# Optimization experiments

Hardware: AMD Instinct MI355X
Metric: run time of the kernel (lower is better)

The kernel has to match this reference:

```python
import jax, jax.numpy as jnp
import numpy as np

NUM_LAYERS = 3
CH = 8            # dynamic head channels
CIN = 8           # mask-branch feature channels
MASK_OUT_STRIDE = 4
WEIGHT_NUMS = [(CIN + 2) * CH, CH * CH, CH * 1]
BIAS_NUMS = [CH, CH, 1]
NUM_GEN_PARAMS = sum(WEIGHT_NUMS) + sum(BIAS_NUMS)  # 169


def compute_locations(h, w, stride):
    # FCOS-style pixel center locations, x-coordinate first: (H*W, 2)
    sx = jnp.arange(w, dtype=jnp.float32) * stride + stride // 2
    sy = jnp.arange(h, dtype=jnp.float32) * stride + stride // 2
    yy, xx = jnp.meshgrid(sy, sx, indexing='ij')
    return jnp.stack([xx.reshape(-1), yy.reshape(-1)], axis=1)


def _resize_axis_align_corners(x, factor, axis):
    # Bilinear, align_corners=True, out_size = factor*(in_size-1)+1.
    # Source coords are exactly j/factor, so interpolation weights are static.
    s = x.shape[axis] - 1
    j = jnp.arange(factor * s + 1)
    i0 = j // factor
    i1 = jnp.minimum(i0 + 1, s)
    frac = (j % factor).astype(x.dtype) / factor
    shp = [1] * x.ndim
    shp[axis] = -1
    frac = frac.reshape(shp)
    return jnp.take(x, i0, axis=axis) * (1 - frac) + jnp.take(x, i1, axis=axis) * frac


def aligned_bilinear(t, factor):
    if factor == 1:
        return t
    h, w = t.shape[2], t.shape[3]
    t = jnp.pad(t, ((0, 0), (0, 0), (0, 1), (0, 1)), mode='edge')   # replicate pad bottom/right
    t = _resize_axis_align_corners(t, factor, 2)                     # -> factor*h + 1
    t = _resize_axis_align_corners(t, factor, 3)                     # -> factor*w + 1
    p = factor // 2
    t = jnp.pad(t, ((0, 0), (0, 0), (p, 0), (p, 0)), mode='edge')    # replicate pad top/left
    return t[:, :, :factor * h, :factor * w]


def parse_params(params):
    # params: (n_inst, 169) -> per-instance weights/biases of the 3 1x1 conv layers
    n = params.shape[0]
    idx = np.cumsum(WEIGHT_NUMS + BIAS_NUMS)[:-1]
    w0, w1, w2, b0, b1, b2 = jnp.split(params, idx, axis=1)
    w0 = w0.reshape(n, CH, CIN + 2)
    w1 = w1.reshape(n, CH, CH)
    w2 = w2.reshape(n, 1, CH)
    b2 = b2.reshape(n, 1)
    return (w0, w1, w2), (b0, b1, b2)


def dynamic_mask_head(mask_feats, mask_head_params, locations, im_inds, fpn_levels, sizes_of_interest, mask_feat_stride):
    N, C, H, W = mask_feats.shape
    n_inst = mask_head_params.shape[0]
    locs = compute_locations(H, W, mask_feat_stride)                 # (HW, 2)
    rel = locations[:, None, :] - locs[None, :, :]                   # (n, HW, 2)
    rel = jnp.transpose(rel, (0, 2, 1))                              # (n, 2, HW)
    soi = sizes_of_interest[fpn_levels]                              # (n,)
    rel = (rel / soi[:, None, None]).astype(mask_feats.dtype)
    feats = mask_feats[im_inds].reshape(n_inst, CIN, H * W)          # gather per-instance image feats
    x = jnp.concatenate([rel, feats], axis=1)                        # (n, CIN+2, HW)
    (w0, w1, w2), (b0, b1, b2) = parse_params(mask_head_params)
    # grouped 1x1 convs (groups = n_inst) == per-instance small matmuls
    x = jax.nn.relu(jnp.einsum('noi,nip->nop', w0, x) + b0[:, :, None])
    x = jax.nn.relu(jnp.einsum('noi,nip->nop', w1, x) + b1[:, :, None])
    x = jnp.einsum('noi,nip->nop', w2, x) + b2[:, :, None]           # (n, 1, HW)
    logits = x.reshape(n_inst, 1, H, W)
    logits = aligned_bilinear(logits, mask_feat_stride // MASK_OUT_STRIDE)
    return jax.nn.sigmoid(logits)


def setup_inputs() -> dict:
    key = jax.random.key(0)
    k1, k2, k3, k4, k5 = jax.random.split(key, 5)
    N, H, W, n_inst = 2, 136, 200, 128
    mask_feats = jax.random.normal(k1, (N, CIN, H, W), dtype=jnp.float32)
    mask_head_params = jax.random.normal(k2, (n_inst, NUM_GEN_PARAMS), dtype=jnp.float32) * 0.1
    locations = jax.random.uniform(k3, (n_inst, 2), dtype=jnp.float32) * 1600.0
    im_inds = jax.random.randint(k4, (n_inst,), 0, N)
    fpn_levels = jax.random.randint(k5, (n_inst,), 0, 5)
    sizes_of_interest = jnp.array([64.0, 128.0, 256.0, 512.0, 1024.0], dtype=jnp.float32)
    return {"mask_feats": mask_feats, "mask_head_params": mask_head_params, "locations": locations,
            "im_inds": im_inds, "fpn_levels": fpn_levels, "sizes_of_interest": sizes_of_interest,
            "mask_feat_stride": 8}


def reference(mask_feats, mask_head_params, locations, im_inds, fpn_levels, sizes_of_interest, mask_feat_stride):
    return dynamic_mask_head(mask_feats, mask_head_params, locations, im_inds, fpn_levels,
                             sizes_of_interest, mask_feat_stride)
```

## Files before the change

### kernel.cpp

```cpp
#include <hip/hip_runtime.h>
#include <math.h>

typedef __fp16 h2 __attribute__((ext_vector_type(2)));

#define H_IN   136
#define W_IN   200
#define HWP    (H_IN * W_IN)
#define OH     272
#define OW     400
#define RB     8
#define NSTRIP 17
#define LROWS  (RB + 1)
#define CH     8
#define CIN    8
#define NPARAM 169
#define NEG_LOG2E (-1.4426950408889634f)



__device__ __forceinline__ h2 pkrtz(float a, float b) {
    return __builtin_amdgcn_cvt_pkrtz(a, b);
}

__global__ __launch_bounds__(256, 3) void mask_head_fused(
    const float* __restrict__ mask_feats,
    const float* __restrict__ params,
    const float* __restrict__ locations,
    const int*   __restrict__ im_inds,
    const int*   __restrict__ fpn_levels,
    const float* __restrict__ soi_tab,
    float* __restrict__ out)
{
    __shared__ h2    sW[NPARAM];
    __shared__ float T[LROWS][W_IN];

    const int inst = blockIdx.y;
    const int r0   = blockIdx.x * RB;
    const int tid  = threadIdx.x;

    const float* P = params + inst * NPARAM;
    if (tid < NPARAM) {
        float w = P[tid];
        if ((tid >= 144 && tid < 152) || tid == 168) w *= NEG_LOG2E;
        const __fp16 hw = (__fp16)w;
        h2 v; v.x = hw; v.y = hw;
        sW[tid] = v;
    }

    const float loc_x   = locations[2 * inst];
    const float loc_y   = locations[2 * inst + 1];
    const float inv_soi = 1.0f / soi_tab[fpn_levels[inst]];
    const float* F = mask_feats + (size_t)im_inds[inst] * (CIN * HWP);
    float* O = out + (size_t)inst * (OH * OW);
    __syncthreads();

    if (tid < LROWS * (W_IN / 8)) {
        const int k = tid / 25;
        const int c = (tid - k * 25) * 8;
        const int r = min(max(r0 - 1 + k, 0), H_IN - 1);

        h2 f[CIN][4];
        #pragma unroll
        for (int ch = 0; ch < CIN; ++ch) {
            const float* q = F + ch * HWP + r * W_IN + c;
            const float4 A = *(const float4*)q;
            const float4 B = *(const float4*)(q + 4);
            f[ch][0] = pkrtz(A.x, A.y); f[ch][1] = pkrtz(A.z, A.w);
            f[ch][2] = pkrtz(B.x, B.y); f[ch][3] = pkrtz(B.z, B.w);
        }

        const float ry  = (loc_y - (float)(r * 8 + 4)) * inv_soi;
        const float dx  = -8.0f * inv_soi;
        const float rx0 = (loc_x - (float)(c * 8 + 4)) * inv_soi;
        h2 rxh[4];
        #pragma unroll
        for (int s = 0; s < 4; ++s)
            rxh[s] = pkrtz(rx0 + (float)(2 * s) * dx, rx0 + (float)(2 * s + 1) * dx);
        const h2 ryh = pkrtz(ry, ry);
        const h2 z2  = {(__fp16)0.0f, (__fp16)0.0f};

        h2 h0[CH][4];
        #pragma unroll
        for (int o = 0; o < CH; ++o) {
            const h2 base = __builtin_elementwise_fma(sW[o * 10 + 1], ryh, sW[152 + o]);
            const h2 wx = sW[o * 10];
            h2 a[4];
            #pragma unroll
            for (int s = 0; s < 4; ++s) a[s] = __builtin_elementwise_fma(wx, rxh[s], base);
            #pragma unroll
            for (int i = 0; i < CIN; ++i) {
                const h2 w = sW[o * 10 + 2 + i];
                #pragma unroll
                for (int s = 0; s < 4; ++s) a[s] = __builtin_elementwise_fma(w, f[i][s], a[s]);
            }
            #pragma unroll
            for (int s = 0; s < 4; ++s) h0[o][s] = __builtin_elementwise_max(a[s], z2);
        }

        h2 h1[CH][4];
        #pragma unroll
        for (int o = 0; o < CH; ++o) {
            const h2 b = sW[160 + o];
            h2 a[4] = {b, b, b, b};
            #pragma unroll
            for (int i = 0; i < CH; ++i) {
                const h2 w = sW[80 + o * CH + i];
                #pragma unroll
                for (int s = 0; s < 4; ++s) a[s] = __builtin_elementwise_fma(w, h0[i][s], a[s]);
            }
            #pragma unroll
            for (int s = 0; s < 4; ++s) h1[o][s] = __builtin_elementwise_max(a[s], z2);
        }

        const h2 b2 = sW[168];
        h2 t[4] = {b2, b2, b2, b2};
        #pragma unroll
        for (int i = 0; i < CH; ++i) {
            const h2 w = sW[144 + i];
            #pragma unroll
            for (int s = 0; s < 4; ++s) t[s] = __builtin_elementwise_fma(w, h1[i][s], t[s]);
        }

        *(float4*)&T[k][c] = make_float4((float)t[0].x, (float)t[0].y,
                                         (float)t[1].x, (float)t[1].y);
        *(float4*)&T[k][c + 4] = make_float4((float)t[2].x, (float)t[2].y,
                                             (float)t[3].x, (float)t[3].y);
    }
    __syncthreads();

    #pragma unroll
    for (int it = 0; it < 2; ++it) {
        const int s = tid + 256 * it;
        if (s < RB * (W_IN / 4)) {
            const int rpl = s / (W_IN / 4);
            const int t   = s - rpl * (W_IN / 4);
            const int cm  = 4 * t;
            const int cl  = max(cm - 1, 0);

            const float4 mR = *(const float4*)&T[rpl + 1][cm];
            const float4 mQ = *(const float4*)&T[rpl][cm];
            const float  AR = T[rpl + 1][cl];
            const float  AQ = T[rpl][cl];

            const float Aa = 0.5f * (AR + AQ);
            const float Ba = 0.5f * (mR.x + mQ.x);
            const float Ca = 0.5f * (mR.y + mQ.y);
            const float Da = 0.5f * (mR.z + mQ.z);
            const float Ea = 0.5f * (mR.w + mQ.w);

            float4 s0, s1, s2, s3;
            s0.x = __builtin_amdgcn_rcpf(1.0f + __builtin_amdgcn_exp2f(0.5f * (Aa + Ba)));
            s0.y = __builtin_amdgcn_rcpf(1.0f + __builtin_amdgcn_exp2f(Ba));
            s0.z = __builtin_amdgcn_rcpf(1.0f + __builtin_amdgcn_exp2f(0.5f * (Ba + Ca)));
            s0.w = __builtin_amdgcn_rcpf(1.0f + __builtin_amdgcn_exp2f(Ca));
            s1.x = __builtin_amdgcn_rcpf(1.0f + __builtin_amdgcn_exp2f(0.5f * (Ca + Da)));
            s1.y = __builtin_amdgcn_rcpf(1.0f + __builtin_amdgcn_exp2f(Da));
            s1.z = __builtin_amdgcn_rcpf(1.0f + __builtin_amdgcn_exp2f(0.5f * (Da + Ea)));
            s1.w = __builtin_amdgcn_rcpf(1.0f + __builtin_amdgcn_exp2f(Ea));

            s2.x = __builtin_amdgcn_rcpf(1.0f + __builtin_amdgcn_exp2f(0.5f * (AR + mR.x)));
            s2.y = __builtin_amdgcn_rcpf(1.0f + __builtin_amdgcn_exp2f(mR.x));
            s2.z = __builtin_amdgcn_rcpf(1.0f + __builtin_amdgcn_exp2f(0.5f * (mR.x + mR.y)));
            s2.w = __builtin_amdgcn_rcpf(1.0f + __builtin_amdgcn_exp2f(mR.y));
            s3.x = __builtin_amdgcn_rcpf(1.0f + __builtin_amdgcn_exp2f(0.5f * (mR.y + mR.z)));
            s3.y = __builtin_amdgcn_rcpf(1.0f + __builtin_amdgcn_exp2f(mR.z));
            s3.z = __builtin_amdgcn_rcpf(1.0f + __builtin_amdgcn_exp2f(0.5f * (mR.z + mR.w)));
            s3.w = __builtin_amdgcn_rcpf(1.0f + __builtin_amdgcn_exp2f(mR.w));

            float* O0 = O + (size_t)(2 * (r0 + rpl)) * OW + 8 * t;
            *(float4*)(O0)          = s0;
            *(float4*)(O0 + 4)      = s1;
            *(float4*)(O0 + OW)     = s2;
            *(float4*)(O0 + OW + 4) = s3;
        }
    }
}

extern "C" void kernel_launch(void* const* d_in, const int* in_sizes, int n_in,
                              void* d_out, int out_size, void* d_ws, size_t ws_size,
                              hipStream_t stream) {
    const float* mask_feats = (const float*)d_in[0];
    const float* params     = (const float*)d_in[1];
    const float* locations  = (const float*)d_in[2];
    const int*   im_inds    = (const int*)d_in[3];
    const int*   fpn_levels = (const int*)d_in[4];
    const float* soi_tab    = (const float*)d_in[5];

    const int n_inst = in_sizes[1] / NPARAM;
    dim3 grid(NSTRIP, n_inst);
    mask_head_fused<<<grid, 256, 0, stream>>>(
        mask_feats, params, locations, im_inds, fpn_levels, soi_tab, (float*)d_out);
}
```

Measured before the change: 26.21 us.

## Use taller 17-row strips with two rows per thread in the MLP stage

The row strip per block grows from 8 to 17 rows, which halves the number of blocks and cuts the halo-row recompute overhead from 9/8 to 18/17. In the MLP stage each thread now evaluates two input rows, so 225 threads cover 18 rows and the shared-weight reads are amortised over twice the pixels. The upsample/sigmoid loop becomes a strided loop with unroll disabled. The cost is roughly double the register demand per thread under launch bounds (256,3), which risks spills, plus fewer blocks to spread across the GPU.

```diff
diff --git a/kernel.cpp b/kernel.cpp
--- a/kernel.cpp
+++ b/kernel.cpp
@@ -8,14 +8,13 @@
 #define HWP    (H_IN * W_IN)
 #define OH     272
 #define OW     400
-#define RB     8
-#define NSTRIP 17
+#define RB     17
+#define NSTRIP 8
 #define LROWS  (RB + 1)
 #define CH     8
 #define CIN    8
 #define NPARAM 169
 #define NEG_LOG2E (-1.4426950408889634f)
-
 
 
 __device__ __forceinline__ h2 pkrtz(float a, float b) {
@@ -54,125 +53,157 @@
     float* O = out + (size_t)inst * (OH * OW);
     __syncthreads();
 
-    if (tid < LROWS * (W_IN / 8)) {
-        const int k = tid / 25;
-        const int c = (tid - k * 25) * 8;
-        const int r = min(max(r0 - 1 + k, 0), H_IN - 1);
-
-        h2 f[CIN][4];
+    if (tid < 9 * 25) {
+        const int q  = tid / 25;
+        const int c  = (tid - q * 25) * 8;
+        const int rA = min(max(r0 - 1 + 2 * q, 0), H_IN - 1);
+        const int rB = min(r0 + 2 * q, H_IN - 1);
+
+        h2 fA[CIN][4], fB[CIN][4];
         #pragma unroll
         for (int ch = 0; ch < CIN; ++ch) {
-            const float* q = F + ch * HWP + r * W_IN + c;
-            const float4 A = *(const float4*)q;
-            const float4 B = *(const float4*)(q + 4);
-            f[ch][0] = pkrtz(A.x, A.y); f[ch][1] = pkrtz(A.z, A.w);
-            f[ch][2] = pkrtz(B.x, B.y); f[ch][3] = pkrtz(B.z, B.w);
-        }
-
-        const float ry  = (loc_y - (float)(r * 8 + 4)) * inv_soi;
+            const float* qa = F + ch * HWP + rA * W_IN + c;
+            const float* qb = F + ch * HWP + rB * W_IN + c;
+            const float4 A0 = *(const float4*)qa;
+            const float4 A1 = *(const float4*)(qa + 4);
+            const float4 B0 = *(const float4*)qb;
+            const float4 B1 = *(const float4*)(qb + 4);
+            fA[ch][0] = pkrtz(A0.x, A0.y); fA[ch][1] = pkrtz(A0.z, A0.w);
+            fA[ch][2] = pkrtz(A1.x, A1.y); fA[ch][3] = pkrtz(A1.z, A1.w);
+            fB[ch][0] = pkrtz(B0.x, B0.y); fB[ch][1] = pkrtz(B0.z, B0.w);
+            fB[ch][2] = pkrtz(B1.x, B1.y); fB[ch][3] = pkrtz(B1.z, B1.w);
+        }
+
         const float dx  = -8.0f * inv_soi;
         const float rx0 = (loc_x - (float)(c * 8 + 4)) * inv_soi;
         h2 rxh[4];
         #pragma unroll
         for (int s = 0; s < 4; ++s)
             rxh[s] = pkrtz(rx0 + (float)(2 * s) * dx, rx0 + (float)(2 * s + 1) * dx);
-        const h2 ryh = pkrtz(ry, ry);
+        const float ryAf = (loc_y - (float)(rA * 8 + 4)) * inv_soi;
+        const float ryBf = (loc_y - (float)(rB * 8 + 4)) * inv_soi;
+        const h2 ryA = pkrtz(ryAf, ryAf);
+        const h2 ryB = pkrtz(ryBf, ryBf);
         const h2 z2  = {(__fp16)0.0f, (__fp16)0.0f};
 
-        h2 h0[CH][4];
+        h2 h0A[CH][4], h0B[CH][4];
         #pragma unroll
         for (int o = 0; o < CH; ++o) {
-            const h2 base = __builtin_elementwise_fma(sW[o * 10 + 1], ryh, sW[152 + o]);
+            const h2 b0 = sW[152 + o];
+            const h2 wy = sW[o * 10 + 1];
             const h2 wx = sW[o * 10];
-            h2 a[4];
-            #pragma unroll
-            for (int s = 0; s < 4; ++s) a[s] = __builtin_elementwise_fma(wx, rxh[s], base);
+            const h2 baseA = __builtin_elementwise_fma(wy, ryA, b0);
+            const h2 baseB = __builtin_elementwise_fma(wy, ryB, b0);
+            h2 aA[4], aB[4];
+            #pragma unroll
+            for (int s = 0; s < 4; ++s) {
+                aA[s] = __builtin_elementwise_fma(wx, rxh[s], baseA);
+                aB[s] = __builtin_elementwise_fma(wx, rxh[s], baseB);
+            }
             #pragma unroll
             for (int i = 0; i < CIN; ++i) {
                 const h2 w = sW[o * 10 + 2 + i];
                 #pragma unroll
-                for (int s = 0; s < 4; ++s) a[s] = __builtin_elementwise_fma(w, f[i][s], a[s]);
-            }
-            #pragma unroll
-            for (int s = 0; s < 4; ++s) h0[o][s] = __builtin_elementwise_max(a[s], z2);
-        }
-
-        h2 h1[CH][4];
+                for (int s = 0; s < 4; ++s) {
+                    aA[s] = __builtin_elementwise_fma(w, fA[i][s], aA[s]);
+                    aB[s] = __builtin_elementwise_fma(w, fB[i][s], aB[s]);
+                }
+            }
+            #pragma unroll
+            for (int s = 0; s < 4; ++s) {
+                h0A[o][s] = __builtin_elementwise_max(aA[s], z2);
+                h0B[o][s] = __builtin_elementwise_max(aB[s], z2);
+            }
+        }
+
+        h2 h1A[CH][4], h1B[CH][4];
         #pragma unroll
         for (int o = 0; o < CH; ++o) {
             const h2 b = sW[160 + o];
-            h2 a[4] = {b, b, b, b};
+            h2 aA[4] = {b, b, b, b};
+            h2 aB[4] = {b, b, b, b};
             #pragma unroll
             for (int i = 0; i < CH; ++i) {
                 const h2 w = sW[80 + o * CH + i];
                 #pragma unroll
-                for (int s = 0; s < 4; ++s) a[s] = __builtin_elementwise_fma(w, h0[i][s], a[s]);
-            }
-            #pragma unroll
-            for (int s = 0; s < 4; ++s) h1[o][s] = __builtin_elementwise_max(a[s], z2);
+                for (int s = 0; s < 4; ++s) {
+                    aA[s] = __builtin_elementwise_fma(w, h0A[i][s], aA[s]);
+                    aB[s] = __builtin_elementwise_fma(w, h0B[i][s], aB[s]);
+                }
+            }
+            #pragma unroll
+            for (int s = 0; s < 4; ++s) {
+                h1A[o][s] = __builtin_elementwise_max(aA[s], z2);
+                h1B[o][s] = __builtin_elementwise_max(aB[s], z2);
+            }
         }
 
         const h2 b2 = sW[168];
-        h2 t[4] = {b2, b2, b2, b2};
+        h2 tA[4] = {b2, b2, b2, b2};
+        h2 tB[4] = {b2, b2, b2, b2};
         #pragma unroll
         for (int i = 0; i < CH; ++i) {
             const h2 w = sW[144 + i];
             #pragma unroll
-            for (int s = 0; s < 4; ++s) t[s] = __builtin_elementwise_fma(w, h1[i][s], t[s]);
-        }
-
-        *(float4*)&T[k][c] = make_float4((float)t[0].x, (float)t[0].y,
-                                         (float)t[1].x, (float)t[1].y);
-        *(float4*)&T[k][c + 4] = make_float4((float)t[2].x, (float)t[2].y,
-                                             (float)t[3].x, (float)t[3].y);
+            for (int s = 0; s < 4; ++s) {
+                tA[s] = __builtin_elementwise_fma(w, h1A[i][s], tA[s]);
+                tB[s] = __builtin_elementwise_fma(w, h1B[i][s], tB[s]);
+            }
+        }
+
+        *(float4*)&T[2 * q][c]     = make_float4((float)tA[0].x, (float)tA[0].y,
+                                                 (float)tA[1].x, (float)tA[1].y);
+        *(float4*)&T[2 * q][c + 4] = make_float4((float)tA[2].x, (float)tA[2].y,
+                                                 (float)tA[3].x, (float)tA[3].y);
+        *(float4*)&T[2 * q + 1][c]     = make_float4((float)tB[0].x, (float)tB[0].y,
+                                                     (float)tB[1].x, (float)tB[1].y);
+        *(float4*)&T[2 * q + 1][c + 4] = make_float4((float)tB[2].x, (float)tB[2].y,
+                                                     (float)tB[3].x, (float)tB[3].y);
     }
     __syncthreads();
 
-    #pragma unroll
-    for (int it = 0; it < 2; ++it) {
-        const int s = tid + 256 * it;
-        if (s < RB * (W_IN / 4)) {
-            const int rpl = s / (W_IN / 4);
-            const int t   = s - rpl * (W_IN / 4);
-            const int cm  = 4 * t;
-            const int cl  = max(cm - 1, 0);
-
-            const float4 mR = *(const float4*)&T[rpl + 1][cm];
-            const float4 mQ = *(const float4*)&T[rpl][cm];
-            const float  AR = T[rpl + 1][cl];
-            const float  AQ = T[rpl][cl];
-
-            const float Aa = 0.5f * (AR + AQ);
-            const float Ba = 0.5f * (mR.x + mQ.x);
-            const float Ca = 0.5f * (mR.y + mQ.y);
-            const float Da = 0.5f * (mR.z + mQ.z);
-            const float Ea = 0.5f * (mR.w + mQ.w);
-
-            float4 s0, s1, s2, s3;
-            s0.x = __builtin_amdgcn_rcpf(1.0f + __builtin_amdgcn_exp2f(0.5f * (Aa + Ba)));
-            s0.y = __builtin_amdgcn_rcpf(1.0f + __builtin_amdgcn_exp2f(Ba));
-            s0.z = __builtin_amdgcn_rcpf(1.0f + __builtin_amdgcn_exp2f(0.5f * (Ba + Ca)));
-            s0.w = __builtin_amdgcn_rcpf(1.0f + __builtin_amdgcn_exp2f(Ca));
-            s1.x = __builtin_amdgcn_rcpf(1.0f + __builtin_amdgcn_exp2f(0.5f * (Ca + Da)));
-            s1.y = __builtin_amdgcn_rcpf(1.0f + __builtin_amdgcn_exp2f(Da));
-            s1.z = __builtin_amdgcn_rcpf(1.0f + __builtin_amdgcn_exp2f(0.5f * (Da + Ea)));
-            s1.w = __builtin_amdgcn_rcpf(1.0f + __builtin_amdgcn_exp2f(Ea));
-
-            s2.x = __builtin_amdgcn_rcpf(1.0f + __builtin_amdgcn_exp2f(0.5f * (AR + mR.x)));
-            s2.y = __builtin_amdgcn_rcpf(1.0f + __builtin_amdgcn_exp2f(mR.x));
-            s2.z = __builtin_amdgcn_rcpf(1.0f + __builtin_amdgcn_exp2f(0.5f * (mR.x + mR.y)));
-            s2.w = __builtin_amdgcn_rcpf(1.0f + __builtin_amdgcn_exp2f(mR.y));
-            s3.x = __builtin_amdgcn_rcpf(1.0f + __builtin_amdgcn_exp2f(0.5f * (mR.y + mR.z)));
-            s3.y = __builtin_amdgcn_rcpf(1.0f + __builtin_amdgcn_exp2f(mR.z));
-            s3.z = __builtin_amdgcn_rcpf(1.0f + __builtin_amdgcn_exp2f(0.5f * (mR.z + mR.w)));
-            s3.w = __builtin_amdgcn_rcpf(1.0f + __builtin_amdgcn_exp2f(mR.w));
-
-            float* O0 = O + (size_t)(2 * (r0 + rpl)) * OW + 8 * t;
-            *(float4*)(O0)          = s0;
-            *(float4*)(O0 + 4)      = s1;
-            *(float4*)(O0 + OW)     = s2;
-            *(float4*)(O0 + OW + 4) = s3;
-        }
+    #pragma unroll 1
+    for (int s = tid; s < RB * (W_IN / 4); s += 256) {
+        const int rpl = s / (W_IN / 4);
+        const int t   = s - rpl * (W_IN / 4);
+        const int cm  = 4 * t;
+        const int cl  = max(cm - 1, 0);
+
+        const float4 mR = *(const float4*)&T[rpl + 1][cm];
+        const float4 mQ = *(const float4*)&T[rpl][cm];
+        const float  AR = T[rpl + 1][cl];
+        const float  AQ = T[rpl][cl];
+
+        const float Aa = 0.5f * (AR + AQ);
+        const float Ba = 0.5f * (mR.x + mQ.x);
+        const float Ca = 0.5f * (mR.y + mQ.y);
+        const float Da = 0.5f * (mR.z + mQ.z);
+        const float Ea = 0.5f * (mR.w + mQ.w);
+
+        float4 s0, s1, s2, s3;
+        s0.x = __builtin_amdgcn_rcpf(1.0f + __builtin_amdgcn_exp2f(0.5f * (Aa + Ba)));
+        s0.y = __builtin_amdgcn_rcpf(1.0f + __builtin_amdgcn_exp2f(Ba));
+        s0.z = __builtin_amdgcn_rcpf(1.0f + __builtin_amdgcn_exp2f(0.5f * (Ba + Ca)));
+        s0.w = __builtin_amdgcn_rcpf(1.0f + __builtin_amdgcn_exp2f(Ca));
+        s1.x = __builtin_amdgcn_rcpf(1.0f + __builtin_amdgcn_exp2f(0.5f * (Ca + Da)));
+        s1.y = __builtin_amdgcn_rcpf(1.0f + __builtin_amdgcn_exp2f(Da));
+        s1.z = __builtin_amdgcn_rcpf(1.0f + __builtin_amdgcn_exp2f(0.5f * (Da + Ea)));
+        s1.w = __builtin_amdgcn_rcpf(1.0f + __builtin_amdgcn_exp2f(Ea));
+
+        s2.x = __builtin_amdgcn_rcpf(1.0f + __builtin_amdgcn_exp2f(0.5f * (AR + mR.x)));
+        s2.y = __builtin_amdgcn_rcpf(1.0f + __builtin_amdgcn_exp2f(mR.x));
+        s2.z = __builtin_amdgcn_rcpf(1.0f + __builtin_amdgcn_exp2f(0.5f * (mR.x + mR.y)));
+        s2.w = __builtin_amdgcn_rcpf(1.0f + __builtin_amdgcn_exp2f(mR.y));
+        s3.x = __builtin_amdgcn_rcpf(1.0f + __builtin_amdgcn_exp2f(0.5f * (mR.y + mR.z)));
+        s3.y = __builtin_amdgcn_rcpf(1.0f + __builtin_amdgcn_exp2f(mR.z));
+        s3.z = __builtin_amdgcn_rcpf(1.0f + __builtin_amdgcn_exp2f(0.5f * (mR.z + mR.w)));
+        s3.w = __builtin_amdgcn_rcpf(1.0f + __builtin_amdgcn_exp2f(mR.w));
+
+        float* O0 = O + (size_t)(2 * (r0 + rpl)) * OW + 8 * t;
+        *(float4*)(O0)          = s0;
+        *(float4*)(O0 + 4)      = s1;
+        *(float4*)(O0 + OW)     = s2;
+        *(float4*)(O0 + OW + 4) = s3;
     }
 }
 
```

Measured after the change: 26.61 us. About the same (+1.5%).
